# Optimization experiments

Measured on AMD Instinct MI355X. Metric: run time of the kernel, lower is better.

Reference implementation:

```python
import jax, jax.numpy as jnp
import numpy as np

OUT = 7          # roi_align output_size
NUM_ANCHORS = 27 # 3 scales x 3 ratios x 3 angles
MAX_PROPOSALS = 100
RPN_STRIDE = 32


def conv2d(x, w, b, stride=1, pad=1):
    y = jax.lax.conv_general_dilated(
        x, w, (stride, stride), [(pad, pad), (pad, pad)],
        dimension_numbers=('NCHW', 'OIHW', 'NCHW'))
    return y + b[None, :, None, None]


def generate_anchors(H, W, stride):
    # matches CustomOrientedRPN.generate_anchors
    sx = np.arange(0, W * stride, stride, dtype=np.float32)
    sy = np.arange(0, H * stride, stride, dtype=np.float32)
    SY, SX = np.meshgrid(sy, sx, indexing='ij')
    shifts = np.stack([SX, SY], axis=-1).reshape(-1, 2)  # [HW,2]
    base = []
    for scale in (32.0, 64.0, 128.0):
        for ratio in (0.5, 1.0, 2.0):
            w = scale * ratio ** 0.5
            h = scale / ratio ** 0.5
            for angle in (0.0, 45.0, 90.0):
                base.append([w, h, angle])
    base = np.array(base, dtype=np.float32)  # [A,3]
    A = base.shape[0]
    anchors = np.concatenate(
        [np.repeat(shifts[:, None, :], A, axis=1),
         np.broadcast_to(base[None], (shifts.shape[0], A, 3))], axis=-1)
    return jnp.asarray(anchors.reshape(-1, 5))  # [HW*A, 5]


def rotated_roi_align(features, boxes, batch_idx):
    # Vectorized version of the per-box affine_grid + grid_sample loop
    # (align_corners=False semantics for both, zero padding for grid_sample).
    B, C, Hf, Wf = features.shape
    lin = (2.0 * jnp.arange(OUT, dtype=features.dtype) + 1.0) / OUT - 1.0
    ys, xs = jnp.meshgrid(lin, lin, indexing='ij')  # [7,7] base grid

    cx, cy, w, h, ang = (boxes[:, i] for i in range(5))
    ar = -ang * jnp.pi / 180.0
    c, s = jnp.cos(ar), jnp.sin(ar)
    t00 = w / Wf * c; t01 = -h / Hf * s; t02 = 2.0 * cx / Wf - 1.0
    t10 = w / Wf * s; t11 = h / Hf * c;  t12 = 2.0 * cy / Hf - 1.0
    gx = t00[:, None, None] * xs + t01[:, None, None] * ys + t02[:, None, None]  # [N,7,7]
    gy = t10[:, None, None] * xs + t11[:, None, None] * ys + t12[:, None, None]

    ix = ((gx + 1.0) * Wf - 1.0) / 2.0
    iy = ((gy + 1.0) * Hf - 1.0) / 2.0
    x0 = jnp.floor(ix); y0 = jnp.floor(iy)
    wx = ix - x0;       wy = iy - y0
    x0i = x0.astype(jnp.int32); y0i = y0.astype(jnp.int32)

    def gather(dx, dy, wgt):
        xi = x0i + dx; yi = y0i + dy
        valid = (xi >= 0) & (xi < Wf) & (yi >= 0) & (yi < Hf)
        xc = jnp.clip(xi, 0, Wf - 1)
        yc = jnp.clip(yi, 0, Hf - 1)
        def one(bi, yb, xb):
            return features[bi][:, yb, xb]  # [C,7,7]
        vals = jax.vmap(one)(batch_idx, yc, xc)  # [N,C,7,7]
        return vals * (wgt * valid)[:, None, :, :]

    return (gather(0, 0, (1 - wx) * (1 - wy)) + gather(1, 0, wx * (1 - wy)) +
            gather(0, 1, (1 - wx) * wy) + gather(1, 1, wx * wy))


def setup_inputs() -> dict:
    key = jax.random.key(0)
    ks = jax.random.split(key, 20)

    def w(k, shape):
        fan_in = int(np.prod(shape[1:]))
        return jax.random.normal(k, shape, jnp.float32) / np.sqrt(fan_in)

    C = 256; A = NUM_ANCHORS; NC = 5
    return {
        'images': jax.random.normal(ks[0], (8, 3, 1024, 1024), jnp.float32),
        'backbone_w': w(ks[1], (C, 3, 3, 3)),   'backbone_b': jnp.zeros((C,), jnp.float32),
        'rpn_conv_w': w(ks[2], (256, C, 3, 3)), 'rpn_conv_b': jnp.zeros((256,), jnp.float32),
        'obj_w': w(ks[3], (A, 256, 1, 1)),      'obj_b': jnp.zeros((A,), jnp.float32),
        'delta_w': w(ks[4], (A * 5, 256, 1, 1)) * 0.1, 'delta_b': jnp.zeros((A * 5,), jnp.float32),
        'fc1_w': w(ks[5], (1024, C * OUT * OUT)), 'fc1_b': jnp.zeros((1024,), jnp.float32),
        'fc2_w': w(ks[6], (1024, 1024)),          'fc2_b': jnp.zeros((1024,), jnp.float32),
        'cls_w': w(ks[7], (NC, 1024)),            'cls_b': jnp.zeros((NC,), jnp.float32),
        'bbox_w': w(ks[8], (5, 1024)),            'bbox_b': jnp.zeros((5,), jnp.float32),
    }


def reference(images, backbone_w, backbone_b, rpn_conv_w, rpn_conv_b,
              obj_w, obj_b, delta_w, delta_b,
              fc1_w, fc1_b, fc2_w, fc2_b, cls_w, cls_b, bbox_w, bbox_b):
    # backbone (stand-in: single stride-16 conv)
    f = conv2d(images, backbone_w, backbone_b, stride=16, pad=1)  # [B,256,64,64]
    B, C, H, W = f.shape
    # F.interpolate(scale_factor=0.5, bilinear, align_corners=False) == 2x2 mean
    f = f.reshape(B, C, H // 2, 2, W // 2, 2).mean(axis=(3, 5))   # [B,256,32,32]
    Hf, Wf = f.shape[2], f.shape[3]

    # RPN
    t = jax.nn.relu(conv2d(f, rpn_conv_w, rpn_conv_b, 1, 1))
    _logits = conv2d(t, obj_w, obj_b, 1, 0)  # computed as in original (unused downstream)
    deltas = conv2d(t, delta_w, delta_b, 1, 0)  # [B, A*5, Hf, Wf]
    A = NUM_ANCHORS
    deltas = deltas.reshape(B, A, 5, Hf, Wf).transpose(0, 3, 4, 1, 2).reshape(B, -1, 5)

    anchors = generate_anchors(Hf, Wf, RPN_STRIDE)  # [HW*A,5]
    acx, acy, aw, ah, aa = (anchors[:, i] for i in range(5))
    pcx = deltas[:, :, 0] * aw + acx
    pcy = deltas[:, :, 1] * ah + acy
    pw = jnp.exp(deltas[:, :, 2]) * aw
    ph = jnp.exp(deltas[:, :, 3]) * ah
    pa = aa + deltas[:, :, 4]
    proposals = jnp.stack([pcx, pcy, pw, ph, pa], axis=-1)  # [B, HW*A, 5]
    proposals = proposals[:, :MAX_PROPOSALS]                # p[:max_proposals]

    boxes = proposals.reshape(-1, 5)                        # [B*100, 5]
    batch_idx = jnp.repeat(jnp.arange(B), MAX_PROPOSALS)
    pooled = rotated_roi_align(f, boxes, batch_idx)         # [B*100, 256, 7, 7]

    x = pooled.reshape(pooled.shape[0], -1)
    x = jax.nn.relu(x @ fc1_w.T + fc1_b)
    x = jax.nn.relu(x @ fc2_w.T + fc2_b)
    class_logits = x @ cls_w.T + cls_b
    obb_preds = x @ bbox_w.T + bbox_b
    return class_logits, obb_preds
```

## Files before the change

### kernel.cpp

```cpp
#include <hip/hip_runtime.h>
#include <hip/hip_bf16.h>

using bf16 = __hip_bfloat16;

typedef __attribute__((ext_vector_type(8))) short bf16x8;
typedef __attribute__((ext_vector_type(4))) float f32x4;

__device__ __forceinline__ void async16(const void* g, void* l) {
  __builtin_amdgcn_global_load_lds(
      (const __attribute__((address_space(1))) unsigned int*)g,
      (__attribute__((address_space(3))) unsigned int*)l, 16, 0, 0);
}

__device__ __forceinline__ void store_o(float* C, size_t i, float v) { C[i] = v; }
__device__ __forceinline__ void store_o(bf16* C, size_t i, float v) {
  C[i] = __float2bfloat16(v);
}

__device__ __forceinline__ unsigned int pk2(float a, float b) {
  unsigned int ua = __bfloat16_as_ushort(__float2bfloat16(a));
  unsigned int ub = __bfloat16_as_ushort(__float2bfloat16(b));
  return ua | (ub << 16);
}

__global__ __launch_bounds__(256) void k_backbone(const float* __restrict__ img,
    const float* __restrict__ w, const float* __restrict__ bias,
    float* __restrict__ f) {
  __shared__ float wlds[6912];
  __shared__ float patch[432];
  int blk = blockIdx.x;
  int xq = blk & 7, y = (blk >> 3) & 31, b = blk >> 8;
  int x0 = xq * 4;
  int t = threadIdx.x;
  for (int i = t; i < 6912; i += 256) wlds[i] = w[i];
  for (int i = t; i < 432; i += 256) {
    int k27 = i % 27, r = i / 27;
    int sub = r & 3, p = r >> 2;
    int kx = k27 % 3, ky = (k27 / 3) % 3, cin = k27 / 9;
    int sy = sub >> 1, sx = sub & 1;
    int iy = (2 * y + sy) * 16 - 1 + ky;
    int ix = (2 * (x0 + p) + sx) * 16 - 1 + kx;
    float v = 0.f;
    if (iy >= 0 && ix >= 0)
      v = img[((size_t)(b * 3 + cin) * 1024 + iy) * 1024 + ix];
    patch[i] = v;
  }
  __syncthreads();
  int c = t;
  float wr[27];
#pragma unroll
  for (int k = 0; k < 27; ++k) wr[k] = wlds[c * 27 + k];
  float bs = bias[c];
#pragma unroll
  for (int p = 0; p < 4; ++p) {
    float acc = 0.f;
#pragma unroll
    for (int sub = 0; sub < 4; ++sub)
#pragma unroll
      for (int k = 0; k < 27; ++k)
        acc += patch[(p * 4 + sub) * 27 + k] * wr[k];
    f[(size_t)((b * 32 + y) * 32 + x0 + p) * 256 + c] = acc * 0.25f + bs;
  }
}

__global__ __launch_bounds__(256) void k_rpn(const float* __restrict__ f,
    const float* __restrict__ rpn_w, float* __restrict__ part) {
  int p = blockIdx.x;
  int kc = blockIdx.y;
  int x = p & 3, b = p >> 2;
  __shared__ float fpl[6][16];
  int tid = threadIdx.x;
  if (tid < 96) {
    int cin2 = tid & 15;
    int rc = tid >> 4;
    int row = rc / 3, col = rc % 3;
    int xc = x - 1 + col;
    float v = 0.f;
    if (xc >= 0)
      v = f[((size_t)(b * 32 + row) * 32 + xc) * 256 + kc * 16 + cin2];
    fpl[rc][cin2] = v;
  }
  __syncthreads();
  int c = tid;
  const float* wbase = rpn_w + (size_t)c * 2304 + kc * 144;
  float acc = 0.f;
#pragma unroll
  for (int cin2 = 0; cin2 < 16; ++cin2) {
    const float* wp = wbase + cin2 * 9;
    acc += fpl[0][cin2] * wp[3] + fpl[1][cin2] * wp[4]
         + fpl[2][cin2] * wp[5] + fpl[3][cin2] * wp[6]
         + fpl[4][cin2] * wp[7] + fpl[5][cin2] * wp[8];
  }
  part[((size_t)kc * 32 + p) * 256 + c] = acc;
}

__global__ __launch_bounds__(512) void k_delta(const float* __restrict__ part,
    const float* __restrict__ rpn_b,
    const float* __restrict__ dw, const float* __restrict__ db,
    float* __restrict__ boxes) {
  int p = blockIdx.x;
  int x = p & 3, b = p >> 2;
  __shared__ float tbuf[256];
  __shared__ float dvals[135];
  int tid = threadIdx.x;
  if (tid < 256) {
    float s = rpn_b[tid];
#pragma unroll
    for (int kc = 0; kc < 16; ++kc)
      s += part[((size_t)kc * 32 + p) * 256 + tid];
    tbuf[tid] = fmaxf(s, 0.f);
  }
  __syncthreads();
  if (tid < 270) {
    int o = tid >> 1, half = tid & 1;
    const float* wp = dw + (size_t)o * 256 + half * 128;
    const float* tp = tbuf + half * 128;
    float s0 = 0.f, s1 = 0.f, s2 = 0.f, s3 = 0.f;
#pragma unroll 8
    for (int k = 0; k < 128; k += 4) {
      s0 += tp[k]     * wp[k];
      s1 += tp[k + 1] * wp[k + 1];
      s2 += tp[k + 2] * wp[k + 2];
      s3 += tp[k + 3] * wp[k + 3];
    }
    float s = (s0 + s1) + (s2 + s3);
    s += __shfl_xor(s, 1, 64);
    if (half == 0) dvals[o] = s + db[o];
  }
  __syncthreads();
  if (tid < 27) {
    int i = x * 27 + tid;
    if (i < 100) {
      int a = tid;
      int si = a / 9, ri = (a / 3) % 3, ai = a % 3;
      float scale = 32.f * (float)(1 << si);
      float sr = (ri == 0) ? 0.70710678118654752f : (ri == 1 ? 1.0f : 1.41421356237309505f);
      float aw = scale * sr, ah = scale / sr;
      float aang = 45.f * (float)ai;
      float acx = 32.f * (float)x, acy = 0.f;
      float* bx = boxes + (size_t)(b * 100 + i) * 5;
      bx[0] = dvals[a * 5 + 0] * aw + acx;
      bx[1] = dvals[a * 5 + 1] * ah + acy;
      bx[2] = expf(dvals[a * 5 + 2]) * aw;
      bx[3] = expf(dvals[a * 5 + 3]) * ah;
      bx[4] = aang + dvals[a * 5 + 4];
    }
  }
}

__global__ __launch_bounds__(256) void k_roialign(const float* __restrict__ f,
    const float* __restrict__ boxes, bf16* __restrict__ pooled) {
  int n = blockIdx.x;
  int b = n / 100;
  __shared__ int six[49], siy[49];
  __shared__ float swx[49], swy[49];
  __shared__ float pool_s[12544];
  int tid = threadIdx.x;
  if (tid < 49) {
    float cx = boxes[n * 5 + 0], cy = boxes[n * 5 + 1];
    float w = boxes[n * 5 + 2], h = boxes[n * 5 + 3], ang = boxes[n * 5 + 4];
    float ar = -ang * 0.017453292519943295f;
    float cc = cosf(ar), ss = sinf(ar);
    float t00 = w * (1.f / 32.f) * cc, t01 = -h * (1.f / 32.f) * ss;
    float t02 = cx * (2.f / 32.f) - 1.f;
    float t10 = w * (1.f / 32.f) * ss, t11 = h * (1.f / 32.f) * cc;
    float t12 = cy * (2.f / 32.f) - 1.f;
    int py = tid / 7, px = tid - py * 7;
    float lx = (2.f * px + 1.f) * (1.f / 7.f) - 1.f;
    float ly = (2.f * py + 1.f) * (1.f / 7.f) - 1.f;
    float gx = t00 * lx + t01 * ly + t02;
    float gy = t10 * lx + t11 * ly + t12;
    float ix = ((gx + 1.f) * 32.f - 1.f) * 0.5f;
    float iy = ((gy + 1.f) * 32.f - 1.f) * 0.5f;
    float x0 = floorf(ix), y0 = floorf(iy);
    six[tid] = (int)x0; siy[tid] = (int)y0;
    swx[tid] = ix - x0; swy[tid] = iy - y0;
  }
  __syncthreads();
  const float* fb = f + (size_t)b * 262144;
  int c = tid;
#pragma unroll 7
  for (int bin = 0; bin < 49; ++bin) {
    int x0 = six[bin], y0 = siy[bin];
    float wx = swx[bin], wy = swy[bin];
    bool x0ok = (x0 >= 0) & (x0 < 32), x1ok = (x0 + 1 >= 0) & (x0 + 1 < 32);
    bool y0ok = (y0 >= 0) & (y0 < 32), y1ok = (y0 + 1 >= 0) & (y0 + 1 < 32);
    int x0c = min(max(x0, 0), 31), x1c = min(max(x0 + 1, 0), 31);
    int y0c = min(max(y0, 0), 31), y1c = min(max(y0 + 1, 0), 31);
    float w00 = (x0ok && y0ok) ? (1.f - wx) * (1.f - wy) : 0.f;
    float w01 = (x1ok && y0ok) ? wx * (1.f - wy) : 0.f;
    float w10 = (x0ok && y1ok) ? (1.f - wx) * wy : 0.f;
    float w11 = (x1ok && y1ok) ? wx * wy : 0.f;
    float acc = fb[(y0c * 32 + x0c) * 256 + c] * w00
              + fb[(y0c * 32 + x1c) * 256 + c] * w01
              + fb[(y1c * 32 + x0c) * 256 + c] * w10
              + fb[(y1c * 32 + x1c) * 256 + c] * w11;
    pool_s[c * 49 + bin] = acc;
  }
  __syncthreads();
  uint2* po = (uint2*)(pooled + (size_t)n * 12544);
  for (int k = tid; k < 3136; k += 256) {
    f32x4 v = *(const f32x4*)&pool_s[k * 4];
    uint2 o; o.x = pk2(v[0], v[1]); o.y = pk2(v[2], v[3]);
    po[k] = o;
  }
}

__global__ __launch_bounds__(256) void k_cvtz(const float* __restrict__ s1,
    const float* __restrict__ s2, uint2* __restrict__ d1,
    uint2* __restrict__ d2, f32x4* __restrict__ Pz) {
  const int N1 = 3211264;
  const int N2 = 262144;
  const int NZ = 204800;
  int stride = gridDim.x * 256;
  for (int j = blockIdx.x * 256 + threadIdx.x; j < N1 + N2 + NZ; j += stride) {
    if (j < N1) {
      float4 v = ((const float4*)s1)[j];
      uint2 o; o.x = pk2(v.x, v.y); o.y = pk2(v.z, v.w);
      d1[j] = o;
    } else if (j < N1 + N2) {
      int i = j - N1;
      float4 v = ((const float4*)s2)[i];
      uint2 o; o.x = pk2(v.x, v.y); o.y = pk2(v.z, v.w);
      d2[i] = o;
    } else {
      Pz[j - N1 - N2] = (f32x4){0.f, 0.f, 0.f, 0.f};
    }
  }
}

__global__ __launch_bounds__(256) void k_gemm_bb(
    const unsigned short* __restrict__ A, const unsigned short* __restrict__ B,
    float* __restrict__ P, int M, int N, int K, int KC, int zmul, int zoff) {
  int b = blockIdx.x;
  int xcd = b & 7, t2 = b >> 3;
  int z = zmul * xcd + zoff;
  int kbeg = z * KC;
  if (kbeg >= K) return;
  int kend = kbeg + KC; if (kend > K) kend = K;
  int n0 = (t2 & 7) * 128;
  int m0 = (t2 >> 3) * 128;

  __shared__ unsigned short As[2][128 * 64];
  __shared__ unsigned short Bs[2][128 * 64];
  int t = threadIdx.x;
  int wv = t >> 6, ln = t & 63;
  int quad = ln >> 4, l15 = ln & 15;
  int wm = wv >> 1, wn = wv & 1;

  int srow = ln >> 3;
  int sg = (ln & 7) ^ srow;
  const unsigned short* Ap[4];
#pragma unroll
  for (int q = 0; q < 4; ++q) {
    int r = m0 + q * 32 + wv * 8 + srow;
    if (r > M - 1) r = M - 1;
    Ap[q] = A + (size_t)r * K + sg * 8;
  }
  const unsigned short* Bp[4];
#pragma unroll
  for (int c = 0; c < 4; ++c) {
    int r = n0 + wv * 32 + c * 8 + srow;
    Bp[c] = B + (size_t)r * K + sg * 8;
  }

  f32x4 acc[4][4];
#pragma unroll
  for (int mf = 0; mf < 4; ++mf)
#pragma unroll
    for (int nf = 0; nf < 4; ++nf) acc[mf][nf] = (f32x4){0.f, 0.f, 0.f, 0.f};

#pragma unroll
  for (int q = 0; q < 4; ++q)
    async16(Ap[q] + kbeg, &As[0][q * 2048 + wv * 512]);
#pragma unroll
  for (int c = 0; c < 4; ++c)
    async16(Bp[c] + kbeg, &Bs[0][wv * 2048 + c * 512]);

  int cur = 0;
  for (int k0 = kbeg; k0 < kend; k0 += 64) {
    int k1 = k0 + 64;
    if (k1 < kend) {
#pragma unroll
      for (int q = 0; q < 4; ++q)
        async16(Ap[q] + k1, &As[cur ^ 1][q * 2048 + wv * 512]);
#pragma unroll
      for (int c = 0; c < 4; ++c)
        async16(Bp[c] + k1, &Bs[cur ^ 1][wv * 2048 + c * 512]);
      asm volatile("s_waitcnt vmcnt(8)" ::: "memory");
    } else {
      asm volatile("s_waitcnt vmcnt(0)" ::: "memory");
    }
    __builtin_amdgcn_s_barrier();
    __builtin_amdgcn_sched_barrier(0);
#pragma unroll
    for (int ks = 0; ks < 2; ++ks) {
      bf16x8 a[4];
#pragma unroll
      for (int mf = 0; mf < 4; ++mf) {
        int row = wm * 64 + mf * 16 + l15;
        a[mf] = *(const bf16x8*)&As[cur][row * 64 + (((ks * 4 + quad) ^ (l15 & 7)) * 8)];
      }
#pragma unroll
      for (int nf = 0; nf < 4; ++nf) {
        int brow = wn * 64 + nf * 16 + l15;
        bf16x8 b2 = *(const bf16x8*)&Bs[cur][brow * 64 + (((ks * 4 + quad) ^ (l15 & 7)) * 8)];
#pragma unroll
        for (int mf = 0; mf < 4; ++mf)
          acc[mf][nf] = __builtin_amdgcn_mfma_f32_16x16x32_bf16(a[mf], b2, acc[mf][nf], 0, 0, 0);
      }
    }
    __builtin_amdgcn_sched_barrier(0);
    asm volatile("" ::: "memory");
    __builtin_amdgcn_s_barrier();
    cur ^= 1;
  }
#pragma unroll
  for (int nf = 0; nf < 4; ++nf) {
    int n = n0 + wn * 64 + nf * 16 + l15;
#pragma unroll
    for (int mf = 0; mf < 4; ++mf) {
#pragma unroll
      for (int r = 0; r < 4; ++r) {
        int m = m0 + wm * 64 + mf * 16 + quad * 4 + r;
        if (m < M) atomicAdd(&P[(size_t)m * N + n], acc[mf][nf][r]);
      }
    }
  }
}

template <typename OutT, bool RZ>
__global__ __launch_bounds__(256) void k_bias_relu(float* __restrict__ P,
    const float* __restrict__ bias, OutT* __restrict__ C, int MN, int N) {
  int i = blockIdx.x * 256 + threadIdx.x;
  if (i * 4 >= MN) return;
  f32x4 s = *(const f32x4*)(P + (size_t)i * 4);
  int n = (i * 4) % N;
#pragma unroll
  for (int u = 0; u < 4; ++u)
    store_o(C, (size_t)i * 4 + u, fmaxf(s[u] + bias[n + u], 0.f));
  if (RZ) *(f32x4*)(P + (size_t)i * 4) = (f32x4){0.f, 0.f, 0.f, 0.f};
}

__global__ __launch_bounds__(640) void k_heads(const float* __restrict__ P,
    const float* __restrict__ fc2_b,
    const float* __restrict__ cls_w, const float* __restrict__ cls_b,
    const float* __restrict__ bbox_w, const float* __restrict__ bbox_b,
    float* __restrict__ out) {
  __shared__ float xr[1024];
  int n = blockIdx.x;
  for (int i = threadIdx.x; i < 1024; i += 640)
    xr[i] = fmaxf(P[(size_t)n * 1024 + i] + fc2_b[i], 0.f);
  __syncthreads();
  int wave = threadIdx.x >> 6;
  int lane = threadIdx.x & 63;
  const float* w = (wave < 5) ? (cls_w + (size_t)wave * 1024)
                              : (bbox_w + (size_t)(wave - 5) * 1024);
  float s = 0.f;
  for (int k = lane; k < 1024; k += 64) s += xr[k] * w[k];
  for (int off = 32; off; off >>= 1) s += __shfl_down(s, off, 64);
  if (lane == 0) {
    int o = (wave < 5) ? wave : wave - 5;
    float bias = (wave < 5) ? cls_b[o] : bbox_b[o];
    int base = (wave < 5) ? 0 : 4000;
    out[base + n * 5 + o] = s + bias;
  }
}

extern "C" void kernel_launch(void* const* d_in, const int* in_sizes, int n_in,
                              void* d_out, int out_size, void* d_ws, size_t ws_size,
                              hipStream_t stream) {
  const float* images     = (const float*)d_in[0];
  const float* backbone_w = (const float*)d_in[1];
  const float* backbone_b = (const float*)d_in[2];
  const float* rpn_w      = (const float*)d_in[3];
  const float* rpn_b      = (const float*)d_in[4];
  const float* delta_w    = (const float*)d_in[7];
  const float* delta_b    = (const float*)d_in[8];
  const float* fc1_w      = (const float*)d_in[9];
  const float* fc1_b      = (const float*)d_in[10];
  const float* fc2_w      = (const float*)d_in[11];
  const float* fc2_b      = (const float*)d_in[12];
  const float* cls_w      = (const float*)d_in[13];
  const float* cls_b      = (const float*)d_in[14];
  const float* bbox_w     = (const float*)d_in[15];
  const float* bbox_b     = (const float*)d_in[16];

  char* ws = (char*)d_ws;
  bf16*  bw1    = (bf16*) ws;
  float* f      = (float*)ws;
  float* boxes  = (float*)(ws + 25690112);
  bf16*  pooled = (bf16*) (ws + 25706496);
  bf16*  x1     = (bf16*) (ws + 45776896);
  float* P      = (float*)(ws + 47415296);
  bf16*  bw2    = (bf16*) (ws + 50692096);
  float* rpart  = P;

  k_backbone<<<2048, 256, 0, stream>>>(images, backbone_w, backbone_b, f);
  k_rpn<<<dim3(32, 16), 256, 0, stream>>>(f, rpn_w, rpart);
  k_delta<<<32, 512, 0, stream>>>(rpart, rpn_b, delta_w, delta_b, boxes);
  k_roialign<<<800, 256, 0, stream>>>(f, boxes, pooled);

  k_cvtz<<<2048, 256, 0, stream>>>(fc1_w, fc2_w, (uint2*)bw1, (uint2*)bw2,
                                   (f32x4*)P);

  k_gemm_bb<<<448, 256, 0, stream>>>(
      (const unsigned short*)pooled, (const unsigned short*)bw1, P,
      800, 1024, 12544, 896, 2, 0);
  k_gemm_bb<<<448, 256, 0, stream>>>(
      (const unsigned short*)pooled, (const unsigned short*)bw1, P,
      800, 1024, 12544, 896, 2, 1);
  k_bias_relu<bf16, true><<<800, 256, 0, stream>>>(P, fc1_b, x1, 819200, 1024);

  k_gemm_bb<<<448, 256, 0, stream>>>(
      (const unsigned short*)x1, (const unsigned short*)bw2, P,
      800, 1024, 1024, 128, 1, 0);

  k_heads<<<800, 640, 0, stream>>>(P, fc2_b, cls_w, cls_b, bbox_w, bbox_b,
                                   (float*)d_out);
}
```

Measured before the change: 357.0 us.

## Merge split-K GEMM launches, fold fc2 convert into backbone, remap roialign blocks

The two split-K fc1 GEMM launches become one launch of 896 blocks, with the k-slice derived from the XCD id plus a group index. The fc2 weight conversion and the zeroing of P move into extra blocks appended to the backbone kernel, so k_cvt1 only converts fc1 weights. rpart now lives in the pooled region rather than in P, which avoids a clash with the early zeroing of P. RoI-align blocks are remapped so that consecutive block ids walk across batch images, which spreads feature-map accesses over the XCDs. The aim is fewer launches and better overlap, at the cost of a larger single GEMM grid and possible contention on the atomics into P.

After: 349.9 us. -2.0%, faster.

```diff
diff --git a/kernel.cpp b/kernel.cpp
--- a/kernel.cpp
+++ b/kernel.cpp
@@ -25,10 +25,27 @@
 
 __global__ __launch_bounds__(256) void k_backbone(const float* __restrict__ img,
     const float* __restrict__ w, const float* __restrict__ bias,
-    float* __restrict__ f) {
+    float* __restrict__ f,
+    const float* __restrict__ fc2w, uint2* __restrict__ bw2,
+    f32x4* __restrict__ Pz) {
+  int blk = blockIdx.x;
+  if (blk >= 2048) {
+    const int N2 = 262144;
+    const int NZ = 204800;
+    int stride = 256 * 256;
+    for (int j = (blk - 2048) * 256 + threadIdx.x; j < N2 + NZ; j += stride) {
+      if (j < N2) {
+        float4 v = ((const float4*)fc2w)[j];
+        uint2 o; o.x = pk2(v.x, v.y); o.y = pk2(v.z, v.w);
+        bw2[j] = o;
+      } else {
+        Pz[j - N2] = (f32x4){0.f, 0.f, 0.f, 0.f};
+      }
+    }
+    return;
+  }
   __shared__ float wlds[6912];
   __shared__ float patch[432];
-  int blk = blockIdx.x;
   int xq = blk & 7, y = (blk >> 3) & 31, b = blk >> 8;
   int x0 = xq * 4;
   int t = threadIdx.x;
@@ -150,8 +167,9 @@
 
 __global__ __launch_bounds__(256) void k_roialign(const float* __restrict__ f,
     const float* __restrict__ boxes, bf16* __restrict__ pooled) {
-  int n = blockIdx.x;
-  int b = n / 100;
+  int bid = blockIdx.x;
+  int n = (bid & 7) * 100 + (bid >> 3);
+  int b = bid & 7;
   __shared__ int six[49], siy[49];
   __shared__ float swx[49], swy[49];
   __shared__ float pool_s[12544];
@@ -206,35 +224,24 @@
   }
 }
 
-__global__ __launch_bounds__(256) void k_cvtz(const float* __restrict__ s1,
-    const float* __restrict__ s2, uint2* __restrict__ d1,
-    uint2* __restrict__ d2, f32x4* __restrict__ Pz) {
+__global__ __launch_bounds__(256) void k_cvt1(const float* __restrict__ s1,
+    uint2* __restrict__ d1) {
   const int N1 = 3211264;
-  const int N2 = 262144;
-  const int NZ = 204800;
   int stride = gridDim.x * 256;
-  for (int j = blockIdx.x * 256 + threadIdx.x; j < N1 + N2 + NZ; j += stride) {
-    if (j < N1) {
-      float4 v = ((const float4*)s1)[j];
-      uint2 o; o.x = pk2(v.x, v.y); o.y = pk2(v.z, v.w);
-      d1[j] = o;
-    } else if (j < N1 + N2) {
-      int i = j - N1;
-      float4 v = ((const float4*)s2)[i];
-      uint2 o; o.x = pk2(v.x, v.y); o.y = pk2(v.z, v.w);
-      d2[i] = o;
-    } else {
-      Pz[j - N1 - N2] = (f32x4){0.f, 0.f, 0.f, 0.f};
-    }
+  for (int j = blockIdx.x * 256 + threadIdx.x; j < N1; j += stride) {
+    float4 v = ((const float4*)s1)[j];
+    uint2 o; o.x = pk2(v.x, v.y); o.y = pk2(v.z, v.w);
+    d1[j] = o;
   }
 }
 
 __global__ __launch_bounds__(256) void k_gemm_bb(
     const unsigned short* __restrict__ A, const unsigned short* __restrict__ B,
-    float* __restrict__ P, int M, int N, int K, int KC, int zmul, int zoff) {
+    float* __restrict__ P, int M, int N, int K, int KC) {
   int b = blockIdx.x;
-  int xcd = b & 7, t2 = b >> 3;
-  int z = zmul * xcd + zoff;
+  int xcd = b & 7, j = b >> 3;
+  int g = j / 56, t2 = j - g * 56;
+  int z = xcd + 8 * g;
   int kbeg = z * KC;
   if (kbeg >= K) return;
   int kend = kbeg + KC; if (kend > K) kend = K;
@@ -391,30 +398,27 @@
   float* f      = (float*)ws;
   float* boxes  = (float*)(ws + 25690112);
   bf16*  pooled = (bf16*) (ws + 25706496);
+  float* rpart  = (float*)(ws + 25706496);
   bf16*  x1     = (bf16*) (ws + 45776896);
   float* P      = (float*)(ws + 47415296);
   bf16*  bw2    = (bf16*) (ws + 50692096);
-  float* rpart  = P;
-
-  k_backbone<<<2048, 256, 0, stream>>>(images, backbone_w, backbone_b, f);
+
+  k_backbone<<<2304, 256, 0, stream>>>(images, backbone_w, backbone_b, f,
+                                       fc2_w, (uint2*)bw2, (f32x4*)P);
   k_rpn<<<dim3(32, 16), 256, 0, stream>>>(f, rpn_w, rpart);
   k_delta<<<32, 512, 0, stream>>>(rpart, rpn_b, delta_w, delta_b, boxes);
   k_roialign<<<800, 256, 0, stream>>>(f, boxes, pooled);
 
-  k_cvtz<<<2048, 256, 0, stream>>>(fc1_w, fc2_w, (uint2*)bw1, (uint2*)bw2,
-                                   (f32x4*)P);
-
-  k_gemm_bb<<<448, 256, 0, stream>>>(
+  k_cvt1<<<2048, 256, 0, stream>>>(fc1_w, (uint2*)bw1);
+
+  k_gemm_bb<<<896, 256, 0, stream>>>(
       (const unsigned short*)pooled, (const unsigned short*)bw1, P,
-      800, 1024, 12544, 896, 2, 0);
-  k_gemm_bb<<<448, 256, 0, stream>>>(
-      (const unsigned short*)pooled, (const unsigned short*)bw1, P,
-      800, 1024, 12544, 896, 2, 1);
+      800, 1024, 12544, 896);
   k_bias_relu<bf16, true><<<800, 256, 0, stream>>>(P, fc1_b, x1, 819200, 1024);
 
   k_gemm_bb<<<448, 256, 0, stream>>>(
       (const unsigned short*)x1, (const unsigned short*)bw2, P,
-      800, 1024, 1024, 128, 1, 0);
+      800, 1024, 1024, 128);
 
   k_heads<<<800, 640, 0, stream>>>(P, fc2_b, cls_w, cls_b, bbox_w, bbox_b,
                                    (float*)d_out);
```
